# Performance work log

Measured on AMD Instinct MI355X. Metric: run time of the kernel, lower is better.

## Reference

```python
import jax, jax.numpy as jnp
import numpy as np

E = 1024
H = 16
D = E // H          # head_dim = 64
FF = 4 * E          # SwiGLU hidden = 4096
B, S = 4, 2048


def layer_norm(x, g, b, eps=1e-5):
    mu = jnp.mean(x, axis=-1, keepdims=True)
    var = jnp.var(x, axis=-1, keepdims=True)
    return (x - mu) * jax.lax.rsqrt(var + eps) * g + b


def setup_inputs() -> dict:
    key = jax.random.key(0)
    ks = jax.random.split(key, 16)
    s = 0.02
    return {
        "value": jax.random.normal(ks[0], (B, S, E), jnp.float32),
        "key": jax.random.normal(ks[1], (B, S, E), jnp.float32),
        "query": jax.random.normal(ks[2], (B, S, E), jnp.float32),
        "mask": jnp.ones((B, 1, 1, S), jnp.int32),
        "g1": jnp.ones((E,), jnp.float32),
        "b1": jnp.zeros((E,), jnp.float32),
        "g2": jnp.ones((E,), jnp.float32),
        "b2": jnp.zeros((E,), jnp.float32),
        "Wv": jax.random.normal(ks[3], (D, D), jnp.float32) * s,
        "Wk": jax.random.normal(ks[4], (D, D), jnp.float32) * s,
        "Wq": jax.random.normal(ks[5], (D, D), jnp.float32) * s,
        "Wo": jax.random.normal(ks[6], (E, E), jnp.float32) * s,
        "bo": jnp.zeros((E,), jnp.float32),
        "W12": jax.random.normal(ks[7], (2 * FF, E), jnp.float32) * s,
        "b12": jnp.zeros((2 * FF,), jnp.float32),
        "W3": jax.random.normal(ks[8], (E, FF), jnp.float32) * s,
        "b3": jnp.zeros((E,), jnp.float32),
    }


def attention(v, k, q, mask, Wv, Wk, Wq, Wo, bo):
    N, Sq = q.shape[0], q.shape[1]
    Sk = k.shape[1]
    # split heads; same per-head Linear (weight shared across heads)
    q = q.reshape(N, Sq, H, D) @ Wq.T
    k = k.reshape(N, Sk, H, D) @ Wk.T
    v = v.reshape(N, Sk, H, D) @ Wv.T
    energy = jnp.einsum('nqhd,nkhd->nhqk', q, k)
    # ALiBi: slopes 2^(-alpha*(i+start)), i=1..H, symmetric |i-j| bias
    slopes = 2.0 ** (-1.0 * jnp.arange(1, H + 1, dtype=jnp.float32))
    dist = jnp.abs(jnp.arange(Sq)[:, None] - jnp.arange(Sk)[None, :]).astype(jnp.float32)
    energy = energy - slopes[None, :, None, None] * dist[None, None]
    energy = jnp.where(mask == 0, jnp.float32(-1e4), energy)
    # note: scaled by sqrt(embed_size), not head_dim (faithful to source)
    attn = jax.nn.softmax(energy / jnp.sqrt(jnp.float32(E)), axis=-1)
    out = jnp.einsum('nhqk,nkhd->nqhd', attn, v).reshape(N, Sq, E)
    return out @ Wo.T + bo


def swiglu(x, W12, b12, W3, b3):
    x12 = x @ W12.T + b12
    x1, x2 = jnp.split(x12, 2, axis=-1)
    return (jax.nn.silu(x1) * x2) @ W3.T + b3


def reference(value, key, query, mask, g1, b1, g2, b2, Wv, Wk, Wq, Wo, bo, W12, b12, W3, b3):
    qn = layer_norm(query, g1, b1)
    kn = layer_norm(key, g1, b1)
    vn = layer_norm(value, g1, b1)
    x = attention(vn, kn, qn, mask, Wv, Wk, Wq, Wo, bo)
    x = query + x                      # dropout is identity in eval
    x = layer_norm(x, g2, b2)
    x = swiglu(x, W12, b12, W3, b3)
    # faithful to source: residual from original query, not pre-FFN x
    return query + x
```

## Files before the change

### kernel.cpp

```cpp
#include <hip/hip_runtime.h>
#include <math.h>

#define EDIM 1024
#define HN 16
#define HD 64
#define SEQ 2048
#define BATCH 4
#define FFD 4096
#define NTOK (BATCH*SEQ)

typedef __attribute__((ext_vector_type(8))) short bf16x8;
typedef __attribute__((ext_vector_type(4))) float f32x4;

union BF8 { bf16x8 v; ushort u[8]; };

__device__ __forceinline__ ushort f2bf(float f) {
  unsigned u = __float_as_uint(f);
  u += 0x7FFFu + ((u >> 16) & 1u);
  return (ushort)(u >> 16);
}

__device__ __forceinline__ void gload16(const ushort* g, ushort* l) {
  __builtin_amdgcn_global_load_lds(
      (const __attribute__((address_space(1))) void*)g,
      (__attribute__((address_space(3))) void*)l, 16, 0, 0);
}

__global__ __launch_bounds__(256) void k_f2b(const float* __restrict__ s,
                                             ushort* __restrict__ d, int n4)
{
  const int i = blockIdx.x * 256 + threadIdx.x;
  if (i < n4) {
    float4 v = ((const float4*)s)[i];
    ushort4 o; o.x = f2bf(v.x); o.y = f2bf(v.y); o.z = f2bf(v.z); o.w = f2bf(v.w);
    ((ushort4*)d)[i] = o;
  }
}

__device__ __forceinline__ void proj_stage(const float* __restrict__ Wg,
                                           const float* xlds, float* wbuf,
                                           ushort* __restrict__ outp,
                                           size_t tE, int tid)
{
  for (int idx = tid; idx < HD * HD; idx += 256)
    wbuf[(idx >> 6) * 68 + (idx & 63)] = Wg[idx];
  __syncthreads();
  const int i = tid >> 2;
  const int g = tid & 3;
  const float4* wr = (const float4*)(wbuf + i * 68);
#pragma unroll
  for (int hh = 0; hh < 4; ++hh) {
    const int h = g * 4 + hh;
    const float4* xr = (const float4*)(xlds + h * 68);
    float acc = 0.f;
#pragma unroll
    for (int j4 = 0; j4 < 16; ++j4) {
      float4 w = wr[j4], x = xr[j4];
      acc += w.x * x.x + w.y * x.y + w.z * x.z + w.w * x.w;
    }
    outp[tE + h * 64 + i] = f2bf(acc);
  }
  __syncthreads();
}

__global__ __launch_bounds__(256) void k_ln_qkv(
    const float* __restrict__ qin, const float* __restrict__ kin,
    const float* __restrict__ vin, const float* __restrict__ g1,
    const float* __restrict__ b1, const float* __restrict__ Wq,
    const float* __restrict__ Wk, const float* __restrict__ Wv,
    ushort* __restrict__ qp, ushort* __restrict__ kp, ushort* __restrict__ vp)
{
  __shared__ float xq[HN * 68], xk[HN * 68], xv[HN * 68];
  __shared__ float wbuf[HD * 68];
  __shared__ float red[4][6];
  const int tid = threadIdx.x;
  const size_t tE = (size_t)blockIdx.x * EDIM;

  float4 aq = ((const float4*)(qin + tE))[tid];
  float4 ak = ((const float4*)(kin + tE))[tid];
  float4 av = ((const float4*)(vin + tE))[tid];

  float sq = aq.x + aq.y + aq.z + aq.w;
  float ssq = aq.x * aq.x + aq.y * aq.y + aq.z * aq.z + aq.w * aq.w;
  float sk = ak.x + ak.y + ak.z + ak.w;
  float ssk = ak.x * ak.x + ak.y * ak.y + ak.z * ak.z + ak.w * ak.w;
  float sv = av.x + av.y + av.z + av.w;
  float ssv = av.x * av.x + av.y * av.y + av.z * av.z + av.w * av.w;
#pragma unroll
  for (int off = 32; off; off >>= 1) {
    sq += __shfl_down(sq, off);   ssq += __shfl_down(ssq, off);
    sk += __shfl_down(sk, off);   ssk += __shfl_down(ssk, off);
    sv += __shfl_down(sv, off);   ssv += __shfl_down(ssv, off);
  }
  if ((tid & 63) == 0) {
    const int w = tid >> 6;
    red[w][0] = sq; red[w][1] = ssq; red[w][2] = sk;
    red[w][3] = ssk; red[w][4] = sv; red[w][5] = ssv;
  }
  __syncthreads();
  sq = red[0][0] + red[1][0] + red[2][0] + red[3][0];
  ssq = red[0][1] + red[1][1] + red[2][1] + red[3][1];
  sk = red[0][2] + red[1][2] + red[2][2] + red[3][2];
  ssk = red[0][3] + red[1][3] + red[2][3] + red[3][3];
  sv = red[0][4] + red[1][4] + red[2][4] + red[3][4];
  ssv = red[0][5] + red[1][5] + red[2][5] + red[3][5];

  const float rE = 1.f / EDIM;
  const float muq = sq * rE, muk = sk * rE, muv = sv * rE;
  const float ivq = rsqrtf(ssq * rE - muq * muq + 1e-5f);
  const float ivk = rsqrtf(ssk * rE - muk * muk + 1e-5f);
  const float ivv = rsqrtf(ssv * rE - muv * muv + 1e-5f);

  float4 gg = ((const float4*)g1)[tid];
  float4 bb = ((const float4*)b1)[tid];
  const int j = tid * 4;
  float* dq = xq + (j >> 6) * 68 + (j & 63);
  float* dk = xk + (j >> 6) * 68 + (j & 63);
  float* dv = xv + (j >> 6) * 68 + (j & 63);
  dq[0] = (aq.x - muq) * ivq * gg.x + bb.x;
  dq[1] = (aq.y - muq) * ivq * gg.y + bb.y;
  dq[2] = (aq.z - muq) * ivq * gg.z + bb.z;
  dq[3] = (aq.w - muq) * ivq * gg.w + bb.w;
  dk[0] = (ak.x - muk) * ivk * gg.x + bb.x;
  dk[1] = (ak.y - muk) * ivk * gg.y + bb.y;
  dk[2] = (ak.z - muk) * ivk * gg.z + bb.z;
  dk[3] = (ak.w - muk) * ivk * gg.w + bb.w;
  dv[0] = (av.x - muv) * ivv * gg.x + bb.x;
  dv[1] = (av.y - muv) * ivv * gg.y + bb.y;
  dv[2] = (av.z - muv) * ivv * gg.z + bb.z;
  dv[3] = (av.w - muv) * ivv * gg.w + bb.w;
  __syncthreads();

  proj_stage(Wq, xq, wbuf, qp, tE, tid);
  proj_stage(Wk, xk, wbuf, kp, tE, tid);
  proj_stage(Wv, xv, wbuf, vp, tE, tid);
}

__global__ __launch_bounds__(256) void k_attn_mfma(
    const ushort* __restrict__ qp, const ushort* __restrict__ kp,
    const ushort* __restrict__ vp, const int* __restrict__ maskp,
    ushort* __restrict__ aob)
{
  __shared__ ushort Klds[64 * 76];
  __shared__ ushort Vt[64 * 76];
  __shared__ int Ms[64];
  const int tid = threadIdx.x;
  const int wid = tid >> 6;
  const int lane = tid & 63;
  const int g = lane >> 4;
  const int lq = lane & 15;
  const int qt = blockIdx.x, h = blockIdx.y, b = blockIdx.z;
  const float slope = exp2f(-(float)(h + 1));
  const int q0 = qt * 64 + wid * 16;
  const size_t rowbase = (size_t)b * SEQ;
  const int colh = h * HD;

  BF8 qf[2];
  {
    const ushort* qrow = qp + (rowbase + q0 + lq) * EDIM + colh;
#pragma unroll
    for (int c = 0; c < 2; ++c) {
      *(ushort4*)(&qf[c].u[0]) = *(const ushort4*)(qrow + c * 32 + g * 4);
      *(ushort4*)(&qf[c].u[4]) = *(const ushort4*)(qrow + c * 32 + 16 + g * 4);
    }
  }

  f32x4 O[4];
#pragma unroll
  for (int d = 0; d < 4; ++d) O[d] = (f32x4){0.f, 0.f, 0.f, 0.f};
  float m_run = -1e30f, l_run = 0.f;
  const int qi = q0 + lq;

  for (int kt = 0; kt < SEQ / 64; ++kt) {
    const int kbase = kt * 64;
    __syncthreads();
#pragma unroll
    for (int u = 0; u < 2; ++u) {
      const int f = tid + u * 256;
      const int key = f >> 3, c8 = f & 7;
      const ushort* ks = kp + (rowbase + kbase + key) * EDIM + colh + c8 * 8;
      ushort4 k0v = *(const ushort4*)ks;
      ushort4 k1v = *(const ushort4*)(ks + 4);
      *(ushort4*)(&Klds[key * 76 + c8 * 8]) = k0v;
      *(ushort4*)(&Klds[key * 76 + c8 * 8 + 4]) = k1v;
      const ushort* vs = vp + (rowbase + kbase + key) * EDIM + colh + c8 * 8;
      ushort4 v0 = *(const ushort4*)vs;
      ushort4 v1 = *(const ushort4*)(vs + 4);
      Vt[(c8 * 8 + 0) * 76 + key] = v0.x;
      Vt[(c8 * 8 + 1) * 76 + key] = v0.y;
      Vt[(c8 * 8 + 2) * 76 + key] = v0.z;
      Vt[(c8 * 8 + 3) * 76 + key] = v0.w;
      Vt[(c8 * 8 + 4) * 76 + key] = v1.x;
      Vt[(c8 * 8 + 5) * 76 + key] = v1.y;
      Vt[(c8 * 8 + 6) * 76 + key] = v1.z;
      Vt[(c8 * 8 + 7) * 76 + key] = v1.w;
    }
    if (tid < 64) Ms[tid] = maskp[b * SEQ + kbase + tid];
    __syncthreads();

    f32x4 sT[4];
#pragma unroll
    for (int kb = 0; kb < 4; ++kb) {
      sT[kb] = (f32x4){0.f, 0.f, 0.f, 0.f};
#pragma unroll
      for (int c = 0; c < 2; ++c) {
        BF8 a;
        const ushort* src = &Klds[(kb * 16 + lq) * 76 + c * 32 + g * 4];
        *(ushort4*)(&a.u[0]) = *(const ushort4*)(src);
        *(ushort4*)(&a.u[4]) = *(const ushort4*)(src + 16);
        sT[kb] = __builtin_amdgcn_mfma_f32_16x16x32_bf16(a.v, qf[c].v, sT[kb],
                                                         0, 0, 0);
      }
    }

    float pv[16];
    float mt = -1e30f;
#pragma unroll
    for (int kb = 0; kb < 4; ++kb)
#pragma unroll
      for (int r = 0; r < 4; ++r) {
        const int kloc = kb * 16 + g * 4 + r;
        const float dist = fabsf((float)(qi - (kbase + kloc)));
        const float s = Ms[kloc] ? (sT[kb][r] - slope * dist) * 0.03125f
                                 : -312.5f;
        pv[kb * 4 + r] = s;
        mt = fmaxf(mt, s);
      }
    mt = fmaxf(mt, __shfl_xor(mt, 16));
    mt = fmaxf(mt, __shfl_xor(mt, 32));
    const float mn = fmaxf(m_run, mt);
    const float corr = __expf(m_run - mn);
    m_run = mn;

    float sum = 0.f;
    BF8 pa[2];
#pragma unroll
    for (int idx = 0; idx < 16; ++idx) {
      const float p = __expf(pv[idx] - mn);
      sum += p;
      pa[idx >> 3].u[idx & 7] = f2bf(p);
    }
    sum += __shfl_xor(sum, 16);
    sum += __shfl_xor(sum, 32);
    l_run = l_run * corr + sum;

    float corrO[4];
#pragma unroll
    for (int r = 0; r < 4; ++r) corrO[r] = __shfl(corr, g * 4 + r);
#pragma unroll
    for (int d = 0; d < 4; ++d)
#pragma unroll
      for (int r = 0; r < 4; ++r) O[d][r] *= corrO[r];

#pragma unroll
    for (int d = 0; d < 4; ++d) {
#pragma unroll
      for (int c = 0; c < 2; ++c) {
        BF8 vb;
        const ushort* vsrc = &Vt[(d * 16 + lq) * 76 + c * 32 + g * 4];
        *(ushort4*)(&vb.u[0]) = *(const ushort4*)(vsrc);
        *(ushort4*)(&vb.u[4]) = *(const ushort4*)(vsrc + 16);
        O[d] = __builtin_amdgcn_mfma_f32_16x16x32_bf16(pa[c].v, vb.v, O[d],
                                                       0, 0, 0);
      }
    }
  }

  float linv[4];
#pragma unroll
  for (int r = 0; r < 4; ++r) linv[r] = 1.f / __shfl(l_run, g * 4 + r);
#pragma unroll
  for (int d = 0; d < 4; ++d)
#pragma unroll
    for (int r = 0; r < 4; ++r)
      aob[(rowbase + q0 + g * 4 + r) * EDIM + colh + d * 16 + lq] =
          f2bf(O[d][r] * linv[r]);
}

__global__ __launch_bounds__(256) void k_gemm_bf(
    const ushort* __restrict__ A, const ushort* __restrict__ W,
    const float* __restrict__ bias, const float* __restrict__ resid,
    float* __restrict__ out, int K)
{
  __shared__ __align__(16) ushort As[128 * 32];
  __shared__ __align__(16) ushort Bs[128 * 32];
  const int tid = threadIdx.x;
  const int wid = tid >> 6, lane = tid & 63;
  const int g = lane >> 4, lq = lane & 15;
  const int m0 = blockIdx.y * 128, n0 = blockIdx.x * 128;
  const int wr = wid >> 1, wc = wid & 1;
  const int srow = lane >> 2;
  const int scol = (lane & 3) * 8;

  f32x4 acc[4][4];
#pragma unroll
  for (int mi = 0; mi < 4; ++mi)
#pragma unroll
    for (int ni = 0; ni < 4; ++ni) acc[mi][ni] = (f32x4){0.f, 0.f, 0.f, 0.f};

  for (int k0 = 0; k0 < K; k0 += 32) {
    __syncthreads();
#pragma unroll
    for (int c = 0; c < 2; ++c) {
      const int r = wid * 32 + c * 16;
      gload16(A + (size_t)(m0 + r + srow) * K + k0 + scol, &As[r * 32]);
      gload16(W + (size_t)(n0 + r + srow) * K + k0 + scol, &Bs[r * 32]);
    }
    __syncthreads();

    BF8 af[4], bf[4];
#pragma unroll
    for (int i = 0; i < 4; ++i) {
      af[i].v = *(const bf16x8*)(&As[(wr * 64 + i * 16 + lq) * 32 + g * 8]);
      bf[i].v = *(const bf16x8*)(&Bs[(wc * 64 + i * 16 + lq) * 32 + g * 8]);
    }
#pragma unroll
    for (int mi = 0; mi < 4; ++mi)
#pragma unroll
      for (int ni = 0; ni < 4; ++ni)
        acc[mi][ni] = __builtin_amdgcn_mfma_f32_16x16x32_bf16(
            af[mi].v, bf[ni].v, acc[mi][ni], 0, 0, 0);
  }

#pragma unroll
  for (int mi = 0; mi < 4; ++mi)
#pragma unroll
    for (int ni = 0; ni < 4; ++ni) {
      const int n = n0 + wc * 64 + ni * 16 + lq;
      const float bv = bias[n];
#pragma unroll
      for (int r = 0; r < 4; ++r) {
        const int m = m0 + wr * 64 + mi * 16 + g * 4 + r;
        out[(size_t)m * EDIM + n] =
            acc[mi][ni][r] + bv + resid[(size_t)m * EDIM + n];
      }
    }
}

__global__ __launch_bounds__(256) void k_ln(
    const float* __restrict__ x, const float* __restrict__ g,
    const float* __restrict__ bb, ushort* __restrict__ y)
{
  __shared__ float red[4][2];
  const int tid = threadIdx.x;
  const size_t tE = (size_t)blockIdx.x * EDIM;
  float4 v = ((const float4*)(x + tE))[tid];
  float s = v.x + v.y + v.z + v.w;
  float ss = v.x * v.x + v.y * v.y + v.z * v.z + v.w * v.w;
#pragma unroll
  for (int off = 32; off; off >>= 1) {
    s += __shfl_down(s, off); ss += __shfl_down(ss, off);
  }
  if ((tid & 63) == 0) { red[tid >> 6][0] = s; red[tid >> 6][1] = ss; }
  __syncthreads();
  s = red[0][0] + red[1][0] + red[2][0] + red[3][0];
  ss = red[0][1] + red[1][1] + red[2][1] + red[3][1];
  const float mu = s * (1.f / EDIM);
  const float inv = rsqrtf(ss * (1.f / EDIM) - mu * mu + 1e-5f);
  float4 gg = ((const float4*)g)[tid];
  float4 b4 = ((const float4*)bb)[tid];
  ushort4 o;
  o.x = f2bf((v.x - mu) * inv * gg.x + b4.x);
  o.y = f2bf((v.y - mu) * inv * gg.y + b4.y);
  o.z = f2bf((v.z - mu) * inv * gg.z + b4.z);
  o.w = f2bf((v.w - mu) * inv * gg.w + b4.w);
  *(ushort4*)(y + tE + tid * 4) = o;
}

__global__ __launch_bounds__(256) void k_gemm_w12sw(
    const ushort* __restrict__ A, const ushort* __restrict__ W12,
    const float* __restrict__ b12, ushort* __restrict__ hbb)
{
  __shared__ __align__(16) ushort As[128 * 32];
  __shared__ __align__(16) ushort Bs1[64 * 32];
  __shared__ __align__(16) ushort Bs2[64 * 32];
  const int tid = threadIdx.x;
  const int wid = tid >> 6, lane = tid & 63;
  const int g = lane >> 4, lq = lane & 15;
  const int m0 = blockIdx.y * 128, n0 = blockIdx.x * 64;
  const int wr = wid >> 1, wc = wid & 1;
  const int srow = lane >> 2;
  const int scol = (lane & 3) * 8;

  f32x4 acc1[4][2], acc2[4][2];
#pragma unroll
  for (int mi = 0; mi < 4; ++mi)
#pragma unroll
    for (int ni = 0; ni < 2; ++ni) {
      acc1[mi][ni] = (f32x4){0.f, 0.f, 0.f, 0.f};
      acc2[mi][ni] = (f32x4){0.f, 0.f, 0.f, 0.f};
    }

  for (int k0 = 0; k0 < EDIM; k0 += 32) {
    __syncthreads();
    if (wid < 2) {
#pragma unroll
      for (int c = 0; c < 4; ++c) {
        const int r = wid * 64 + c * 16;
        gload16(A + (size_t)(m0 + r + srow) * EDIM + k0 + scol, &As[r * 32]);
      }
    } else if (wid == 2) {
#pragma unroll
      for (int c = 0; c < 4; ++c)
        gload16(W12 + (size_t)(n0 + c * 16 + srow) * EDIM + k0 + scol,
                &Bs1[(c * 16) * 32]);
    } else {
#pragma unroll
      for (int c = 0; c < 4; ++c)
        gload16(W12 + (size_t)(FFD + n0 + c * 16 + srow) * EDIM + k0 + scol,
                &Bs2[(c * 16) * 32]);
    }
    __syncthreads();

    BF8 af[4], bf1[2], bf2[2];
#pragma unroll
    for (int i = 0; i < 4; ++i)
      af[i].v = *(const bf16x8*)(&As[(wr * 64 + i * 16 + lq) * 32 + g * 8]);
#pragma unroll
    for (int i = 0; i < 2; ++i) {
      bf1[i].v = *(const bf16x8*)(&Bs1[(wc * 32 + i * 16 + lq) * 32 + g * 8]);
      bf2[i].v = *(const bf16x8*)(&Bs2[(wc * 32 + i * 16 + lq) * 32 + g * 8]);
    }
#pragma unroll
    for (int mi = 0; mi < 4; ++mi)
#pragma unroll
      for (int ni = 0; ni < 2; ++ni) {
        acc1[mi][ni] = __builtin_amdgcn_mfma_f32_16x16x32_bf16(
            af[mi].v, bf1[ni].v, acc1[mi][ni], 0, 0, 0);
        acc2[mi][ni] = __builtin_amdgcn_mfma_f32_16x16x32_bf16(
            af[mi].v, bf2[ni].v, acc2[mi][ni], 0, 0, 0);
      }
  }

#pragma unroll
  for (int mi = 0; mi < 4; ++mi)
#pragma unroll
    for (int ni = 0; ni < 2; ++ni) {
      const int n = n0 + wc * 32 + ni * 16 + lq;
      const float bv1 = b12[n];
      const float bv2 = b12[FFD + n];
#pragma unroll
      for (int r = 0; r < 4; ++r) {
        const int m = m0 + wr * 64 + mi * 16 + g * 4 + r;
        const float z1 = acc1[mi][ni][r] + bv1;
        const float z2 = acc2[mi][ni][r] + bv2;
        const float h = (z1 / (1.f + __expf(-z1))) * z2;
        hbb[(size_t)m * FFD + n] = f2bf(h);
      }
    }
}

extern "C" void kernel_launch(void* const* d_in, const int* in_sizes, int n_in,
                              void* d_out, int out_size, void* d_ws, size_t ws_size,
                              hipStream_t stream)
{
  const float* value = (const float*)d_in[0];
  const float* key   = (const float*)d_in[1];
  const float* query = (const float*)d_in[2];
  const int*   mask  = (const int*)d_in[3];
  const float* g1 = (const float*)d_in[4];
  const float* b1 = (const float*)d_in[5];
  const float* g2 = (const float*)d_in[6];
  const float* b2 = (const float*)d_in[7];
  const float* Wv = (const float*)d_in[8];
  const float* Wk = (const float*)d_in[9];
  const float* Wq = (const float*)d_in[10];
  const float* Wo = (const float*)d_in[11];
  const float* bo = (const float*)d_in[12];
  const float* W12 = (const float*)d_in[13];
  const float* b12 = (const float*)d_in[14];
  const float* W3  = (const float*)d_in[15];
  const float* b3  = (const float*)d_in[16];
  float* out = (float*)d_out;

  const size_t NE = (size_t)NTOK * EDIM;
  char* w = (char*)d_ws;
  ushort* qp   = (ushort*)w;              w += NE * 2;
  ushort* kp   = (ushort*)w;              w += NE * 2;
  ushort* vp   = (ushort*)w;              w += NE * 2;
  ushort* aob  = (ushort*)w;              w += NE * 2;
  ushort* Wob  = (ushort*)w;              w += (size_t)EDIM * EDIM * 2;
  ushort* W12b = (ushort*)w;              w += (size_t)2 * FFD * EDIM * 2;
  ushort* W3b  = (ushort*)w;              w += (size_t)EDIM * FFD * 2;
  float*  xb   = (float*)w;               w += NE * 4;
  ushort* xnb  = (ushort*)w;              w += NE * 2;
  ushort* hbb  = (ushort*)w;              w += (size_t)NTOK * FFD * 2;

  k_f2b<<<(EDIM * EDIM / 4 + 255) / 256, 256, 0, stream>>>(Wo, Wob,
                                                           EDIM * EDIM / 4);
  k_f2b<<<(2 * FFD * EDIM / 4 + 255) / 256, 256, 0, stream>>>(W12, W12b,
                                                              2 * FFD * EDIM / 4);
  k_f2b<<<(EDIM * FFD / 4 + 255) / 256, 256, 0, stream>>>(W3, W3b,
                                                          EDIM * FFD / 4);
  k_ln_qkv<<<NTOK, 256, 0, stream>>>(query, key, value, g1, b1, Wq, Wk, Wv,
                                     qp, kp, vp);
  k_attn_mfma<<<dim3(SEQ / 64, HN, BATCH), 256, 0, stream>>>(qp, kp, vp, mask,
                                                             aob);
  k_gemm_bf<<<dim3(EDIM / 128, NTOK / 128), 256, 0, stream>>>(aob, Wob, bo,
                                                              query, xb, EDIM);
  k_ln<<<NTOK, 256, 0, stream>>>(xb, g2, b2, xnb);
  k_gemm_w12sw<<<dim3(FFD / 64, NTOK / 128), 256, 0, stream>>>(xnb, W12b, b12,
                                                               hbb);
  k_gemm_bf<<<dim3(EDIM / 128, NTOK / 128), 256, 0, stream>>>(hbb, W3b, b3,
                                                              query, out, FFD);
}
```

Measured before the change: 898.4 us.

## Pre-transpose V globally, use exp2 softmax and skip redundant rescaling in attention

Adds a separate kernel that transposes V per head into a [b,h,d,seq] buffer, so the attention kernel can load V tiles with vectorized 16-byte copies instead of scattered 2-byte LDS stores. Softmax folds the 1/sqrt(E) scale and log2(e) into one constant and uses the hardware exp2. It skips the output rescale when no row maximum increases in the wavefront. Probabilities are converted to bf16 by truncation rather than rounding. This adds an extra kernel launch plus one more read and write of V in global memory, and slightly changes numerics.

```diff
diff --git a/kernel.cpp b/kernel.cpp
--- a/kernel.cpp
+++ b/kernel.cpp
@@ -19,6 +19,15 @@
   u += 0x7FFFu + ((u >> 16) & 1u);
   return (ushort)(u >> 16);
 }
+__device__ __forceinline__ ushort f2bf_trunc(float f) {
+  return (ushort)(__float_as_uint(f) >> 16);
+}
+
+#if __has_builtin(__builtin_amdgcn_exp2f)
+#define EXP2(x) __builtin_amdgcn_exp2f(x)
+#else
+#define EXP2(x) exp2f(x)
+#endif
 
 __device__ __forceinline__ void gload16(const ushort* g, ushort* l) {
   __builtin_amdgcn_global_load_lds(
@@ -136,13 +145,38 @@
   proj_stage(Wv, xv, wbuf, vp, tE, tid);
 }
 
+__global__ __launch_bounds__(256) void k_vtr(const ushort* __restrict__ vp,
+                                             ushort* __restrict__ vt)
+{
+  __shared__ ushort T[64 * 72];
+  const int tid = threadIdx.x;
+  const int kt = blockIdx.x, h = blockIdx.y, b = blockIdx.z;
+  const int kbase = kt * 64;
+  const size_t inbase = ((size_t)b * SEQ + kbase) * EDIM + h * HD;
+#pragma unroll
+  for (int u = 0; u < 2; ++u) {
+    const int f = tid + u * 256;
+    const int key = f >> 3, c8 = f & 7;
+    uint4 v = *(const uint4*)(vp + inbase + (size_t)key * EDIM + c8 * 8);
+    *(uint4*)(&T[key * 72 + c8 * 8]) = v;
+  }
+  __syncthreads();
+  const int d = tid >> 2, kc = tid & 3;
+  ushort o[16];
+#pragma unroll
+  for (int i = 0; i < 16; ++i) o[i] = T[(kc * 16 + i) * 72 + d];
+  ushort* dst = vt + ((size_t)(b * HN + h) * HD + d) * SEQ + kbase + kc * 16;
+  *(uint4*)(dst) = *(uint4*)(&o[0]);
+  *(uint4*)(dst + 8) = *(uint4*)(&o[8]);
+}
+
 __global__ __launch_bounds__(256) void k_attn_mfma(
     const ushort* __restrict__ qp, const ushort* __restrict__ kp,
-    const ushort* __restrict__ vp, const int* __restrict__ maskp,
+    const ushort* __restrict__ vt, const int* __restrict__ maskp,
     ushort* __restrict__ aob)
 {
   __shared__ ushort Klds[64 * 76];
-  __shared__ ushort Vt[64 * 76];
+  __shared__ ushort Vt[64 * 80];
   __shared__ int Ms[64];
   const int tid = threadIdx.x;
   const int wid = tid >> 6;
@@ -150,10 +184,12 @@
   const int g = lane >> 4;
   const int lq = lane & 15;
   const int qt = blockIdx.x, h = blockIdx.y, b = blockIdx.z;
-  const float slope = exp2f(-(float)(h + 1));
+  const float SC2 = 0.04508422f;
+  const float slope2 = exp2f(-(float)(h + 1)) * SC2;
   const int q0 = qt * 64 + wid * 16;
   const size_t rowbase = (size_t)b * SEQ;
   const int colh = h * HD;
+  const size_t vtbase = (size_t)(b * HN + h) * HD * SEQ;
 
   BF8 qf[2];
   {
@@ -177,23 +213,18 @@
 #pragma unroll
     for (int u = 0; u < 2; ++u) {
       const int f = tid + u * 256;
-      const int key = f >> 3, c8 = f & 7;
-      const ushort* ks = kp + (rowbase + kbase + key) * EDIM + colh + c8 * 8;
-      ushort4 k0v = *(const ushort4*)ks;
-      ushort4 k1v = *(const ushort4*)(ks + 4);
-      *(ushort4*)(&Klds[key * 76 + c8 * 8]) = k0v;
-      *(ushort4*)(&Klds[key * 76 + c8 * 8 + 4]) = k1v;
-      const ushort* vs = vp + (rowbase + kbase + key) * EDIM + colh + c8 * 8;
-      ushort4 v0 = *(const ushort4*)vs;
-      ushort4 v1 = *(const ushort4*)(vs + 4);
-      Vt[(c8 * 8 + 0) * 76 + key] = v0.x;
-      Vt[(c8 * 8 + 1) * 76 + key] = v0.y;
-      Vt[(c8 * 8 + 2) * 76 + key] = v0.z;
-      Vt[(c8 * 8 + 3) * 76 + key] = v0.w;
-      Vt[(c8 * 8 + 4) * 76 + key] = v1.x;
-      Vt[(c8 * 8 + 5) * 76 + key] = v1.y;
-      Vt[(c8 * 8 + 6) * 76 + key] = v1.z;
-      Vt[(c8 * 8 + 7) * 76 + key] = v1.w;
+      {
+        const int key = f >> 3, c8 = f & 7;
+        const ushort* ks = kp + (rowbase + kbase + key) * EDIM + colh + c8 * 8;
+        uint4 kv = *(const uint4*)ks;
+        *(uint2*)(&Klds[key * 76 + c8 * 8]) = make_uint2(kv.x, kv.y);
+        *(uint2*)(&Klds[key * 76 + c8 * 8 + 4]) = make_uint2(kv.z, kv.w);
+      }
+      {
+        const int d = f >> 3, c8 = f & 7;
+        const ushort* vs = vt + vtbase + (size_t)d * SEQ + kbase + c8 * 8;
+        *(uint4*)(&Vt[d * 80 + c8 * 8]) = *(const uint4*)vs;
+      }
     }
     if (tid < 64) Ms[tid] = maskp[b * SEQ + kbase + tid];
     __syncthreads();
@@ -221,43 +252,52 @@
       for (int r = 0; r < 4; ++r) {
         const int kloc = kb * 16 + g * 4 + r;
         const float dist = fabsf((float)(qi - (kbase + kloc)));
-        const float s = Ms[kloc] ? (sT[kb][r] - slope * dist) * 0.03125f
-                                 : -312.5f;
+        const float s = Ms[kloc] ? fmaf(sT[kb][r], SC2, -slope2 * dist)
+                                 : -450.84f;
         pv[kb * 4 + r] = s;
         mt = fmaxf(mt, s);
       }
     mt = fmaxf(mt, __shfl_xor(mt, 16));
     mt = fmaxf(mt, __shfl_xor(mt, 32));
-    const float mn = fmaxf(m_run, mt);
-    const float corr = __expf(m_run - mn);
-    m_run = mn;
 
     float sum = 0.f;
     BF8 pa[2];
-#pragma unroll
-    for (int idx = 0; idx < 16; ++idx) {
-      const float p = __expf(pv[idx] - mn);
-      sum += p;
-      pa[idx >> 3].u[idx & 7] = f2bf(p);
+    if (__any(mt > m_run)) {
+      const float mn = fmaxf(m_run, mt);
+      const float corr = EXP2(m_run - mn);
+      m_run = mn;
+#pragma unroll
+      for (int idx = 0; idx < 16; ++idx) {
+        const float p = EXP2(pv[idx] - mn);
+        sum += p;
+        pa[idx >> 3].u[idx & 7] = f2bf_trunc(p);
+      }
+      float corrO[4];
+#pragma unroll
+      for (int r = 0; r < 4; ++r) corrO[r] = __shfl(corr, g * 4 + r);
+#pragma unroll
+      for (int d = 0; d < 4; ++d)
+#pragma unroll
+        for (int r = 0; r < 4; ++r) O[d][r] *= corrO[r];
+      l_run = l_run * corr + 0.f;
+    } else {
+#pragma unroll
+      for (int idx = 0; idx < 16; ++idx) {
+        const float p = EXP2(pv[idx] - m_run);
+        sum += p;
+        pa[idx >> 3].u[idx & 7] = f2bf_trunc(p);
+      }
     }
     sum += __shfl_xor(sum, 16);
     sum += __shfl_xor(sum, 32);
-    l_run = l_run * corr + sum;
-
-    float corrO[4];
-#pragma unroll
-    for (int r = 0; r < 4; ++r) corrO[r] = __shfl(corr, g * 4 + r);
-#pragma unroll
-    for (int d = 0; d < 4; ++d)
-#pragma unroll
-      for (int r = 0; r < 4; ++r) O[d][r] *= corrO[r];
+    l_run += sum;
 
 #pragma unroll
     for (int d = 0; d < 4; ++d) {
 #pragma unroll
       for (int c = 0; c < 2; ++c) {
         BF8 vb;
-        const ushort* vsrc = &Vt[(d * 16 + lq) * 76 + c * 32 + g * 4];
+        const ushort* vsrc = &Vt[(d * 16 + lq) * 80 + c * 32 + g * 4];
         *(ushort4*)(&vb.u[0]) = *(const ushort4*)(vsrc);
         *(ushort4*)(&vb.u[4]) = *(const ushort4*)(vsrc + 16);
         O[d] = __builtin_amdgcn_mfma_f32_16x16x32_bf16(pa[c].v, vb.v, O[d],
@@ -478,6 +518,7 @@
   ushort* qp   = (ushort*)w;              w += NE * 2;
   ushort* kp   = (ushort*)w;              w += NE * 2;
   ushort* vp   = (ushort*)w;              w += NE * 2;
+  ushort* vtb  = (ushort*)w;              w += NE * 2;
   ushort* aob  = (ushort*)w;              w += NE * 2;
   ushort* Wob  = (ushort*)w;              w += (size_t)EDIM * EDIM * 2;
   ushort* W12b = (ushort*)w;              w += (size_t)2 * FFD * EDIM * 2;
@@ -494,7 +535,8 @@
                                                           EDIM * FFD / 4);
   k_ln_qkv<<<NTOK, 256, 0, stream>>>(query, key, value, g1, b1, Wq, Wk, Wv,
                                      qp, kp, vp);
-  k_attn_mfma<<<dim3(SEQ / 64, HN, BATCH), 256, 0, stream>>>(qp, kp, vp, mask,
+  k_vtr<<<dim3(SEQ / 64, HN, BATCH), 256, 0, stream>>>(vp, vtb);
+  k_attn_mfma<<<dim3(SEQ / 64, HN, BATCH), 256, 0, stream>>>(qp, kp, vtb, mask,
                                                              aob);
   k_gemm_bf<<<dim3(EDIM / 128, NTOK / 128), 256, 0, stream>>>(aob, Wob, bo,
                                                               query, xb, EDIM);
```

Measured after the change: 930.5 us. 1.04x slower.
